# Optimization experiments

Hardware: AMD Instinct MI355X
Metric: run time of the kernel (lower is better)

Reference implementation:

```python
import jax, jax.numpy as jnp
import numpy as np

SIGMA = 4.0
KSIZE = 2 * int(4.0 * SIGMA + 0.5) + 1  # 33, as in anomalib's GaussianBlur2d
INPUT_SIZE = (224, 224)
NUM_NEIGHBORS = 9


def avg_pool_4_1_1(x):
    # nn.AvgPool2d(kernel_size=4, stride=1, padding=1), count_include_pad=True -> divide by 16
    s = jax.lax.reduce_window(x, 0.0, jax.lax.add, (1, 1, 4, 4), (1, 1, 1, 1),
                              ((0, 0), (0, 0), (1, 1), (1, 1)))
    return s / 16.0


def gaussian_kernel1d(ksize, sigma):
    x = jnp.arange(ksize, dtype=jnp.float32) - (ksize - 1) / 2.0
    g = jnp.exp(-0.5 * (x / sigma) ** 2)
    return g / jnp.sum(g)


def gaussian_blur(x):
    # separable 33x33 gaussian blur, reflect padding (kornia GaussianBlur2d default)
    k = gaussian_kernel1d(KSIZE, SIGMA)
    pad = KSIZE // 2
    xp = jnp.pad(x, ((0, 0), (0, 0), (pad, pad), (pad, pad)), mode='reflect')
    dn = ('NCHW', 'OIHW', 'NCHW')
    y = jax.lax.conv_general_dilated(xp, k.reshape(1, 1, KSIZE, 1), (1, 1), 'VALID', dimension_numbers=dn)
    y = jax.lax.conv_general_dilated(y, k.reshape(1, 1, 1, KSIZE), (1, 1), 'VALID', dimension_numbers=dn)
    return y


def euclidean_dist(x, y):
    # pairwise L2: x [..., n, d], y [..., m, d] -> [..., n, m]
    x2 = jnp.sum(x * x, axis=-1, keepdims=True)
    y2 = jnp.sum(y * y, axis=-1, keepdims=True)
    d2 = x2 - 2.0 * jnp.matmul(x, jnp.swapaxes(y, -1, -2)) + jnp.swapaxes(y2, -1, -2)
    return jnp.sqrt(jnp.clip(d2, 0.0, None))


def compute_anomaly_score(patch_scores, locations, embedding, memory_bank):
    # PatchCore re-weighting (num_neighbors > 1 branch)
    B, P = patch_scores.shape
    bidx = jnp.arange(B)
    max_patches = jnp.argmax(patch_scores, axis=1)                      # [B]
    feats = embedding.reshape(B, P, -1)[bidx, max_patches]              # [B, C]
    score = patch_scores[bidx, max_patches]                             # [B] s*
    nn_index = locations[bidx, max_patches]                             # [B]
    nn_sample = memory_bank[nn_index]                                   # [B, C]
    d_bank = euclidean_dist(nn_sample, memory_bank)                     # [B, M]
    _, support = jax.lax.top_k(-d_bank, NUM_NEIGHBORS)                  # [B, K] smallest
    support_feats = memory_bank[support]                                # [B, K, C]
    distances = euclidean_dist(feats[:, None, :], support_feats)        # [B, 1, K]
    weights = 1.0 - jnp.exp(score) / jnp.sum(jnp.exp(distances[:, 0, :]), axis=-1)
    return weights * score


def setup_inputs() -> dict:
    key = jax.random.key(0)
    k1, k2, k3 = jax.random.split(key, 3)
    feat_layer2 = jax.random.normal(k1, (8, 512, 28, 28), dtype=jnp.float32)
    feat_layer3 = jax.random.normal(k2, (8, 1024, 14, 14), dtype=jnp.float32)
    memory_bank = jax.random.normal(k3, (32000, 1536), dtype=jnp.float32)
    return {"feat_layer2": feat_layer2, "feat_layer3": feat_layer3, "memory_bank": memory_bank}


def reference(feat_layer2, feat_layer3, memory_bank):
    # feature_pooler = AvgPool2d(4,1,1)
    f2 = avg_pool_4_1_1(feat_layer2)   # [B, 512, 27, 27]
    f3 = avg_pool_4_1_1(feat_layer3)   # [B, 1024, 13, 13]
    B, _, H, W = f2.shape
    # generate_embedding: bilinear upsample layer3 to layer2 size, concat channels
    f3u = jax.image.resize(f3, (B, f3.shape[1], H, W), method='bilinear')
    emb = jnp.concatenate([f2, f3u], axis=1)                            # [B, 1536, 27, 27]
    C = emb.shape[1]
    embedding = jnp.transpose(emb, (0, 2, 3, 1)).reshape(-1, C)         # [B*H*W, C]
    # nearest_neighbors with n_neighbors=1 over the coreset memory bank
    d = euclidean_dist(embedding, memory_bank)                          # [B*H*W, M]
    patch_scores = jnp.min(d, axis=1).reshape(B, -1)
    locations = jnp.argmin(d, axis=1).reshape(B, -1)
    pred_score = compute_anomaly_score(patch_scores, locations, embedding, memory_bank)
    # anomaly map: upsample patch scores to input size + gaussian blur
    pmap = patch_scores.reshape(B, 1, H, W)
    amap = jax.image.resize(pmap, (B, 1, INPUT_SIZE[0], INPUT_SIZE[1]), method='bilinear')
    anomaly_map = gaussian_blur(amap)
    return anomaly_map, pred_score
```

## Files before the change

### kernel.cpp

```cpp
#include <hip/hip_runtime.h>
#include <math.h>

#define NB 8
#define C2 512
#define C3 1024
#define HIN2 28
#define HIN3 14
#define HO2 27
#define HO3 13
#define CC 1536
#define NP (NB*HO2*HO2)
#define NM 32000
#define NKNN 9
#define OH 224
#define AMAP_N (NB*OH*OH)

#define BM 256
#define BN 256
#define BK 64
#define KT (CC/BK)
#define MB_CNT ((NP+BM-1)/BM)
#define NB_CNT (NM/BN)
#define NWG (MB_CNT*NB_CNT)

typedef unsigned long long u64;
typedef unsigned int u32;
typedef __attribute__((ext_vector_type(8))) short bf16x8;
typedef __attribute__((ext_vector_type(4))) float f32x4;

struct GW { float w[33]; };

__device__ __forceinline__ float warp_sum(float v){
  #pragma unroll
  for (int off=32; off; off>>=1) v += __shfl_down(v, off);
  return v;
}

__device__ __forceinline__ ushort f2bf(float f){
  u32 u = __float_as_uint(f);
  u32 r = (u + 0x7FFFu + ((u>>16)&1u)) >> 16;
  return (ushort)r;
}
__device__ __forceinline__ float bf2f(ushort b){
  return __uint_as_float(((u32)b)<<16);
}

#define GLDS(g, l) __builtin_amdgcn_global_load_lds((const __attribute__((address_space(1))) void*)(g), (__attribute__((address_space(3))) void*)(l), 16, 0, 0)
#define WAITVM0() asm volatile("s_waitcnt vmcnt(0)" ::: "memory")
#define SB0() __builtin_amdgcn_sched_barrier(0)
__device__ __forceinline__ void bar_raw(){
  asm volatile("" ::: "memory");
  __builtin_amdgcn_s_barrier();
  asm volatile("" ::: "memory");
}

__global__ __launch_bounds__(256) void k_avgpool2(const float* __restrict__ in, ushort* __restrict__ embB){
  __shared__ float pl[16*789];
  int b = blockIdx.x >> 5, cg = blockIdx.x & 31;
  const float4* src = (const float4*)(in + ((size_t)b*C2 + cg*16)*(HIN2*HIN2));
  for (int idx = threadIdx.x; idx < 16*196; idx += 256){
    int c = idx/196, p4 = idx - c*196;
    float4 v = src[idx];
    float* d = &pl[c*789 + p4*4];
    d[0]=v.x; d[1]=v.y; d[2]=v.z; d[3]=v.w;
  }
  __syncthreads();
  int c = threadIdx.x & 15, g = threadIdx.x >> 4;
  for (int pos = g; pos < HO2*HO2; pos += 16){
    int i = pos/HO2, j = pos - i*HO2;
    const float* p = &pl[c*789];
    float s = 0.f;
    #pragma unroll
    for (int di=0; di<4; ++di){
      int y = i - 1 + di;
      if ((unsigned)y >= HIN2) continue;
      #pragma unroll
      for (int dj=0; dj<4; ++dj){
        int x = j - 1 + dj;
        if ((unsigned)x < HIN2) s += p[y*HIN2 + x];
      }
    }
    embB[((size_t)((b*HO2 + i)*HO2 + j))*CC + cg*16 + c] = f2bf(s * (1.f/16.f));
  }
}

__global__ __launch_bounds__(256) void k_avgpool3(const float* __restrict__ in, float* __restrict__ f3p){
  __shared__ float pl[64*197];
  int b = blockIdx.x >> 4, cg = blockIdx.x & 15;
  const float4* src = (const float4*)(in + ((size_t)b*C3 + cg*64)*(HIN3*HIN3));
  for (int idx = threadIdx.x; idx < 64*49; idx += 256){
    int c = idx/49, p4 = idx - c*49;
    float4 v = src[idx];
    float* d = &pl[c*197 + p4*4];
    d[0]=v.x; d[1]=v.y; d[2]=v.z; d[3]=v.w;
  }
  __syncthreads();
  int c = threadIdx.x & 63, g = threadIdx.x >> 6;
  for (int pos = g; pos < HO3*HO3; pos += 4){
    int i = pos/HO3, j = pos - i*HO3;
    const float* p = &pl[c*197];
    float s = 0.f;
    #pragma unroll
    for (int di=0; di<4; ++di){
      int y = i - 1 + di;
      if ((unsigned)y >= HIN3) continue;
      #pragma unroll
      for (int dj=0; dj<4; ++dj){
        int x = j - 1 + dj;
        if ((unsigned)x < HIN3) s += p[y*HIN3 + x];
      }
    }
    f3p[((size_t)((b*HO3 + i)*HO3 + j))*C3 + cg*64 + c] = s * (1.f/16.f);
  }
}

__global__ void k_upsample3(const float* __restrict__ f3p, ushort* __restrict__ embB){
  int t = blockIdx.x*256 + threadIdx.x;
  if (t >= NB*HO2*HO2*C3) return;
  int c = t % C3; int r = t / C3;
  int ox = r % HO2; r /= HO2;
  int oy = r % HO2; int b = r / HO2;
  float fy = (oy + 0.5f) * (13.f/27.f) - 0.5f;
  float fx = (ox + 0.5f) * (13.f/27.f) - 0.5f;
  int y0 = (int)floorf(fy); float wy = fy - (float)y0;
  int x0 = (int)floorf(fx); float wx = fx - (float)x0;
  int y0c = min(max(y0,0), HO3-1), y1c = min(max(y0+1,0), HO3-1);
  int x0c = min(max(x0,0), HO3-1), x1c = min(max(x0+1,0), HO3-1);
  const float* base = f3p + (size_t)(b*HO3*HO3)*C3;
  float v00 = base[(size_t)(y0c*HO3 + x0c)*C3 + c];
  float v01 = base[(size_t)(y0c*HO3 + x1c)*C3 + c];
  float v10 = base[(size_t)(y1c*HO3 + x0c)*C3 + c];
  float v11 = base[(size_t)(y1c*HO3 + x1c)*C3 + c];
  float v = (1.f-wy)*((1.f-wx)*v00 + wx*v01) + wy*((1.f-wx)*v10 + wx*v11);
  embB[((size_t)((b*HO2 + oy)*HO2 + ox))*CC + C2 + c] = f2bf(v);
}

__global__ void k_bank_prep(const float* __restrict__ bank, ushort* __restrict__ bankB,
                            float* __restrict__ y2){
  int wave = threadIdx.x >> 6, lane = threadIdx.x & 63;
  int r = blockIdx.x*4 + wave;
  if (r >= NM) return;
  const float4* p = (const float4*)(bank + (size_t)r*CC);
  ushort4* q = (ushort4*)(bankB + (size_t)r*CC);
  float s = 0.f;
  #pragma unroll
  for (int it=0; it<6; ++it){
    float4 v = p[it*64 + lane];
    s += v.x*v.x + v.y*v.y + v.z*v.z + v.w*v.w;
    ushort4 o; o.x = f2bf(v.x); o.y = f2bf(v.y); o.z = f2bf(v.z); o.w = f2bf(v.w);
    q[it*64 + lane] = o;
  }
  s = warp_sum(s);
  if (lane==0) y2[r] = s;
}

__global__ void k_rowsumsq_bf(const ushort* __restrict__ src, float* __restrict__ dst, int rows,
                              u64* __restrict__ packed){
  int wave = threadIdx.x >> 6;
  int lane = threadIdx.x & 63;
  int r = blockIdx.x*4 + wave;
  if (r >= rows) return;
  const uint4* p = (const uint4*)(src + (size_t)r*CC);
  float s = 0.f;
  #pragma unroll
  for (int it=0; it<3; ++it){
    uint4 v = p[it*64 + lane];
    u32 ws_[4] = {v.x, v.y, v.z, v.w};
    #pragma unroll
    for (int q=0;q<4;q++){
      float lo = __uint_as_float(ws_[q]<<16);
      float hi = __uint_as_float(ws_[q]&0xFFFF0000u);
      s += lo*lo + hi*hi;
    }
  }
  s = warp_sum(s);
  if (lane==0){ dst[r] = s; packed[r] = ~0ull; }
}

__global__ __launch_bounds__(512, 2) void k_distmin_mfma(
    const ushort* __restrict__ A, const ushort* __restrict__ B,
    const float* __restrict__ x2, const float* __restrict__ y2,
    u64* __restrict__ packed)
{
  __shared__ ushort smem[4*BM*BK];
  ushort* As0 = smem;
  ushort* Bs0 = smem + BM*BK;
  ushort* As1 = smem + 2*BM*BK;
  ushort* Bs1 = smem + 3*BM*BK;

  const int tid = threadIdx.x;
  const int w   = tid >> 6;
  const int l   = tid & 63;
  const int wr  = w >> 2;
  const int wc  = w & 3;
  const int ccol = l & 15;
  const int cgrp = l >> 4;

  int orig = blockIdx.x;
  const int q8 = NWG/8, r8 = NWG%8;
  int xcd = orig & 7, sidx = orig >> 3;
  int wg = (xcd < r8 ? xcd*(q8+1) : r8*(q8+1) + (xcd-r8)*q8) + sidx;
  const int mb = wg % MB_CNT;
  const int nb = wg / MB_CNT;
  const int m0 = mb * BM;
  const int n0 = nb * BN;

  const int rowin = l >> 3;
  const int scol  = (((l&7) ^ rowin) * 8);
  int chA1[2], chA2[2], chB1[2], chB2[2];
  u32 aO1[2], aO2[2], bO1[2], bO2[2];
  u32 lA1[2], lA2[2], lB1[2], lB2[2];
  #pragma unroll
  for (int c=0;c<2;c++){
    chA1[c] = (w<4) ? (2*w+c) : (8+2*w+c);
    chA2[c] = chA1[c] + 8;
    chB1[c] = (w>>1)*8 + (w&1)*2 + c;
    chB2[c] = chB1[c] + 4;
    aO1[c] = (u32)min(m0 + chA1[c]*8 + rowin, NP-1)*CC + scol;
    aO2[c] = (u32)min(m0 + chA2[c]*8 + rowin, NP-1)*CC + scol;
    bO1[c] = (u32)(n0 + chB1[c]*8 + rowin)*CC + scol;
    bO2[c] = (u32)(n0 + chB2[c]*8 + rowin)*CC + scol;
    lA1[c] = (u32)chA1[c]*1024 + l*16;
    lA2[c] = (u32)chA2[c]*1024 + l*16;
    lB1[c] = (u32)chB1[c]*1024 + l*16;
    lB2[c] = (u32)chB2[c]*1024 + l*16;
  }

  const u32 o0 = (u32)((cgrp ^ (ccol & 7)) * 8);
  u32 aRow[8], bRow[4];
  #pragma unroll
  for (int mi=0;mi<8;mi++) aRow[mi] = (u32)(wr*128 + mi*16 + ccol)*BK;
  #pragma unroll
  for (int ni=0;ni<4;ni++) bRow[ni] = (u32)(wc*64 + ni*16 + ccol)*BK;

  f32x4 acc[8][4];
  #pragma unroll
  for (int mi=0;mi<8;mi++)
    #pragma unroll
    for (int ni=0;ni<4;ni++)
      acc[mi][ni] = (f32x4){0.f,0.f,0.f,0.f};

  bf16x8 rA[8][2], rB[4][2];

  #pragma unroll
  for (int c=0;c<2;c++){
    GLDS(A + aO1[c], (char*)As0 + lA1[c]);
    GLDS(A + aO2[c], (char*)As0 + lA2[c]);
    GLDS(B + bO1[c], (char*)Bs0 + lB1[c]);
    GLDS(B + bO2[c], (char*)Bs0 + lB2[c]);
  }
  WAITVM0(); bar_raw(); SB0();
  #pragma unroll
  for (int mi=0;mi<8;mi++)
    #pragma unroll
    for (int ks=0;ks<2;ks++)
      rA[mi][ks] = *(const bf16x8*)&As0[aRow[mi] + (o0 ^ (u32)(ks<<5))];
  #pragma unroll
  for (int ni=0;ni<4;ni++)
    #pragma unroll
    for (int ks=0;ks<2;ks++)
      rB[ni][ks] = *(const bf16x8*)&Bs0[bRow[ni] + (o0 ^ (u32)(ks<<5))];

  #pragma unroll 1
  for (int kt=0; kt<KT; ++kt){
    const u32 kk = (u32)(kt+1)*BK;
    ushort* nA = (kt & 1) ? As0 : As1;
    ushort* nB = (kt & 1) ? Bs0 : Bs1;

    #pragma unroll
    for (int c=0;c<2;c++){
      GLDS(A + aO1[c] + kk, (char*)nA + lA1[c]);
      GLDS(A + aO2[c] + kk, (char*)nA + lA2[c]);
      GLDS(B + bO1[c] + kk, (char*)nB + lB1[c]);
      GLDS(B + bO2[c] + kk, (char*)nB + lB2[c]);
    }
    SB0();

    __builtin_amdgcn_s_setprio(1);
    #pragma unroll
    for (int mi=0;mi<8;mi++)
      #pragma unroll
      for (int ni=0;ni<4;ni++)
        #pragma unroll
        for (int ks=0;ks<2;ks++)
          acc[mi][ni] = __builtin_amdgcn_mfma_f32_16x16x32_bf16(rA[mi][ks], rB[ni][ks], acc[mi][ni], 0, 0, 0);
    __builtin_amdgcn_s_setprio(0);

    WAITVM0();
    bar_raw();
    SB0();

    #pragma unroll
    for (int mi=0;mi<8;mi++)
      #pragma unroll
      for (int ks=0;ks<2;ks++)
        rA[mi][ks] = *(const bf16x8*)&nA[aRow[mi] + (o0 ^ (u32)(ks<<5))];
    #pragma unroll
    for (int ni=0;ni<4;ni++)
      #pragma unroll
      for (int ks=0;ks<2;ks++)
        rB[ni][ks] = *(const bf16x8*)&nB[bRow[ni] + (o0 ^ (u32)(ks<<5))];
  }

  float xv[8][4];
  #pragma unroll
  for (int mi=0;mi<8;mi++)
    #pragma unroll
    for (int r=0;r<4;r++)
      xv[mi][r] = x2[min(m0 + wr*128 + mi*16 + cgrp*4 + r, NP-1)];

  u64 best[8][4];
  #pragma unroll
  for (int mi=0;mi<8;mi++)
    #pragma unroll
    for (int r=0;r<4;r++) best[mi][r] = ~0ull;

  #pragma unroll
  for (int ni=0;ni<4;ni++){
    const int n = n0 + wc*64 + ni*16 + ccol;
    const float yy = y2[n];
    #pragma unroll
    for (int mi=0;mi<8;mi++)
      #pragma unroll
      for (int r=0;r<4;r++){
        float d2 = fmaxf(xv[mi][r] + yy - 2.f*acc[mi][ni][r], 0.f);
        u64 pk = (((u64)__float_as_uint(d2))<<32) | (u32)n;
        if (pk < best[mi][r]) best[mi][r] = pk;
      }
  }

  #pragma unroll
  for (int mi=0;mi<8;mi++)
    #pragma unroll
    for (int r=0;r<4;r++){
      u64 pk = best[mi][r];
      #pragma unroll
      for (int md=1; md<16; md<<=1){
        u64 o = __shfl_xor(pk, md);
        if (o < pk) pk = o;
      }
      const int row = m0 + wr*128 + mi*16 + cgrp*4 + r;
      if (ccol==0 && row < NP) atomicMin(&packed[row], pk);
    }
}

__global__ void k_finalize(const u64* __restrict__ packed, float* __restrict__ patch_d,
                           int* __restrict__ sel_mp, float* __restrict__ sel_score, int* __restrict__ sel_nn){
  int b = blockIdx.x;
  int tid = threadIdx.x;
  __shared__ u64 red[4];
  u64 best = 0;
  for (int p = tid; p < HO2*HO2; p += 256){
    u64 v = packed[b*HO2*HO2 + p];
    float d = sqrtf(__uint_as_float((u32)(v>>32)));
    patch_d[b*HO2*HO2 + p] = d;
    u64 pk = (((u64)__float_as_uint(d))<<32) | (u32)(HO2*HO2 - p);
    if (pk > best) best = pk;
  }
  int lane = tid & 63, w = tid >> 6;
  #pragma unroll
  for (int d=32; d; d>>=1){ u64 o = __shfl_down(best, d); if (o > best) best = o; }
  if (lane==0) red[w] = best;
  __syncthreads();
  if (tid==0){
    u64 bb = red[0];
    for (int q=1;q<4;q++) if (red[q] > bb) bb = red[q];
    int p = HO2*HO2 - (int)(bb & 0xffffffffu);
    sel_mp[b] = p;
    sel_score[b] = __uint_as_float((u32)(bb>>32));
    sel_nn[b] = (int)(packed[b*HO2*HO2 + p] & 0xffffffffu);
  }
}

__device__ __forceinline__ void bf8dec(uint4 v, float* f){
  u32 a[4] = {v.x, v.y, v.z, v.w};
  #pragma unroll
  for (int q=0;q<4;q++){
    f[2*q]   = __uint_as_float(a[q]<<16);
    f[2*q+1] = __uint_as_float(a[q]&0xFFFF0000u);
  }
}

__global__ __launch_bounds__(256) void k_dbank(const ushort* __restrict__ bankB, const float* __restrict__ y2,
    const int* __restrict__ sel_nn, float* __restrict__ d_bank){
  int wave = threadIdx.x >> 6, lane = threadIdx.x & 63;
  int m = blockIdx.x*4 + wave;
  if (m >= NM) return;
  int nn[NB];
  #pragma unroll
  for (int b=0;b<NB;b++) nn[b] = sel_nn[b];
  const uint4* pm = (const uint4*)(bankB + (size_t)m*CC);
  float acc[NB];
  #pragma unroll
  for (int b=0;b<NB;b++) acc[b] = 0.f;
  #pragma unroll
  for (int it=0; it<3; ++it){
    uint4 v = pm[it*64 + lane];
    float vf[8]; bf8dec(v, vf);
    #pragma unroll
    for (int b=0;b<NB;b++){
      uint4 u = ((const uint4*)(bankB + (size_t)nn[b]*CC))[it*64 + lane];
      float uf[8]; bf8dec(u, uf);
      #pragma unroll
      for (int q=0;q<8;q++) acc[b] += vf[q]*uf[q];
    }
  }
  #pragma unroll
  for (int b=0;b<NB;b++){
    float s = warp_sum(acc[b]);
    if (lane==0) d_bank[(size_t)b*NM + m] = fmaxf(y2[nn[b]] + y2[m] - 2.f*s, 0.f);
  }
}

__global__ __launch_bounds__(512) void k_score(const float* __restrict__ d_bank, const float* __restrict__ bank,
    const ushort* __restrict__ embB, const float* __restrict__ x2, const float* __restrict__ y2,
    const int* __restrict__ sel_mp, const float* __restrict__ sel_score, float* __restrict__ out_score){
  int b = blockIdx.x, tid = threadIdx.x;
  __shared__ u64 cand[512*NKNN];
  __shared__ int sel[NKNN];
  __shared__ u64 red[8];
  __shared__ u64 gbest_s;
  __shared__ float fred[8];
  __shared__ float sumexp_s;

  #pragma unroll
  for (int q=0;q<NKNN;q++) cand[tid*NKNN+q] = ~0ull;
  for (int m = tid; m < NM; m += 512){
    float v = d_bank[(size_t)b*NM + m];
    u64 pk = (((u64)__float_as_uint(v))<<32) | (u32)m;
    if (pk < cand[tid*NKNN + NKNN-1]){
      cand[tid*NKNN + NKNN-1] = pk;
      for (int q=NKNN-1; q>0 && cand[tid*NKNN+q] < cand[tid*NKNN+q-1]; --q){
        u64 t = cand[tid*NKNN+q]; cand[tid*NKNN+q] = cand[tid*NKNN+q-1]; cand[tid*NKNN+q-1] = t;
      }
    }
  }
  __syncthreads();
  int lane = tid & 63, w = tid >> 6;
  for (int k=0;k<NKNN;++k){
    u64 mybest = ~0ull;
    #pragma unroll
    for (int q=0;q<NKNN;q++){ u64 v = cand[tid*NKNN+q]; if (v < mybest) mybest = v; }
    u64 rb = mybest;
    #pragma unroll
    for (int d=32; d; d>>=1){ u64 o = __shfl_down(rb, d); if (o < rb) rb = o; }
    if (lane==0) red[w] = rb;
    __syncthreads();
    if (tid==0){
      u64 bb = red[0];
      for (int q=1;q<8;q++) if (red[q] < bb) bb = red[q];
      gbest_s = bb;
      sel[k] = (int)(bb & 0xffffffffu);
    }
    __syncthreads();
    u64 gb = gbest_s;
    #pragma unroll
    for (int q=0;q<NKNN;q++) if (cand[tid*NKNN+q] == gb) cand[tid*NKNN+q] = ~0ull;
    __syncthreads();
  }

  int mp = sel_mp[b];
  const ushort* fv = embB + (size_t)(b*HO2*HO2 + mp)*CC;
  float fx2 = x2[b*HO2*HO2 + mp];
  if (tid==0) sumexp_s = 0.f;
  __syncthreads();
  for (int k=0;k<NKNN;++k){
    const float* sv = bank + (size_t)sel[k]*CC;
    float part = 0.f;
    for (int i = tid; i < CC; i += 512) part += bf2f(fv[i])*sv[i];
    part = warp_sum(part);
    if (lane==0) fred[w] = part;
    __syncthreads();
    if (tid==0){
      float dot = 0.f;
      for (int q=0;q<8;q++) dot += fred[q];
      float d2 = fmaxf(fx2 + y2[sel[k]] - 2.f*dot, 0.f);
      sumexp_s += expf(sqrtf(d2));
    }
    __syncthreads();
  }
  if (tid==0){
    float s = sel_score[b];
    out_score[b] = (1.f - expf(s)/sumexp_s) * s;
  }
}

__global__ void k_maketab(float* __restrict__ T, GW gw){
  int idx = blockIdx.x*256 + threadIdx.x;
  if (idx >= OH*HO2) return;
  int x = idx / HO2, j = idx - x*HO2;
  float s = 0.f;
  #pragma unroll
  for (int k=0;k<33;++k){
    int yy = x + k - 16;
    yy = (yy < 0) ? -yy : yy;
    yy = (yy > OH-1) ? (2*(OH-1) - yy) : yy;
    float fy = (yy + 0.5f) * (27.f/224.f) - 0.5f;
    int y0 = (int)floorf(fy); float wy = fy - (float)y0;
    int j0 = min(max(y0,0), HO2-1), j1 = min(max(y0+1,0), HO2-1);
    float c = ((j==j0)?(1.f-wy):0.f) + ((j==j1)?wy:0.f);
    s += gw.w[k]*c;
  }
  T[idx] = s;
}

__global__ __launch_bounds__(256) void k_amap_fused(const float* __restrict__ patch_d,
    const float* __restrict__ T, float* __restrict__ out){
  __shared__ float Ts[OH*HO2];
  __shared__ float ps[HO2*HO2];
  __shared__ float tmp[HO2*OH];
  int b = blockIdx.x, t = threadIdx.x;
  for (int idx=t; idx<OH*HO2; idx+=256) Ts[idx] = T[idx];
  for (int idx=t; idx<HO2*HO2; idx+=256) ps[idx] = patch_d[b*HO2*HO2+idx];
  __syncthreads();
  for (int idx=t; idx<HO2*OH; idx+=256){
    int i = idx/OH, x = idx - i*OH;
    float s = 0.f;
    #pragma unroll
    for (int j=0;j<HO2;j++) s += ps[i*HO2+j]*Ts[x*HO2+j];
    tmp[i*OH+x] = s;
  }
  __syncthreads();
  for (int idx=t; idx<OH*OH; idx+=256){
    int y = idx/OH, x = idx - y*OH;
    float s = 0.f;
    #pragma unroll
    for (int i=0;i<HO2;i++) s += Ts[y*HO2+i]*tmp[i*OH+x];
    out[(size_t)b*OH*OH + idx] = s;
  }
}

extern "C" void kernel_launch(void* const* d_in, const int* in_sizes, int n_in,
                              void* d_out, int out_size, void* d_ws, size_t ws_size,
                              hipStream_t stream){
  const float* f2   = (const float*)d_in[0];
  const float* f3   = (const float*)d_in[1];
  const float* bank = (const float*)d_in[2];
  float* out = (float*)d_out;

  char* ws = (char*)d_ws;
  size_t off = 0;
  auto alloc = [&](size_t bytes)->char*{ char* p = ws + off; off += (bytes + 255) & ~(size_t)255; return p; };
  ushort* embB    = (ushort*)alloc((size_t)NP*CC*2);
  ushort* bankB   = (ushort*)alloc((size_t)NM*CC*2);
  float* f3p      = (float*)alloc((size_t)NB*HO3*HO3*C3*4);
  float* y2       = (float*)alloc((size_t)NM*4);
  float* x2       = (float*)alloc((size_t)NP*4);
  u64*   packed   = (u64*)  alloc((size_t)NP*8);
  float* patch_d  = (float*)alloc((size_t)NP*4);
  float* d_bank   = (float*)alloc((size_t)NB*NM*4);
  int*   sel_mp   = (int*)  alloc(NB*4);
  float* sel_scr  = (float*)alloc(NB*4);
  int*   sel_nn   = (int*)  alloc(NB*4);
  float* Tmat     = (float*)alloc((size_t)OH*HO2*4);

  GW gw;
  { float s=0.f; for(int i=0;i<33;i++){ float xx=(float)i-16.f; gw.w[i]=expf(-0.5f*(xx/4.f)*(xx/4.f)); s+=gw.w[i]; }
    for(int i=0;i<33;i++) gw.w[i]/=s; }

  k_avgpool2<<<NB*32,256,0,stream>>>(f2, embB);
  k_avgpool3<<<NB*16,256,0,stream>>>(f3, f3p);
  k_upsample3<<<(NB*HO2*HO2*C3+255)/256,256,0,stream>>>(f3p, embB);
  k_bank_prep<<<(NM+3)/4,256,0,stream>>>(bank, bankB, y2);
  k_rowsumsq_bf<<<(NP+3)/4,256,0,stream>>>(embB, x2, NP, packed);
  k_maketab<<<(OH*HO2+255)/256,256,0,stream>>>(Tmat, gw);
  k_distmin_mfma<<<NWG,512,0,stream>>>(embB, bankB, x2, y2, packed);
  k_finalize<<<NB,256,0,stream>>>(packed, patch_d, sel_mp, sel_scr, sel_nn);
  k_dbank<<<(NM+3)/4,256,0,stream>>>(bankB, y2, sel_nn, d_bank);
  k_score<<<NB,512,0,stream>>>(d_bank, bank, embB, x2, y2, sel_mp, sel_scr, out + AMAP_N);
  k_amap_fused<<<NB,256,0,stream>>>(patch_d, Tmat, out);
}
```

Baseline: 941.1 us.

## Split top-9 neighbor search across many blocks and fuse blur table build

The top-9 search over the 32000-entry bank distances moves out of an 8-block kernel into a 256-block partial kernel that keeps per-thread candidates in registers, followed by a small final merge kernel. The Gaussian/bilinear table computation is folded into the anomaly-map kernel, dropping one launch. The GEMM loop also skips the out-of-range prefetch on its last k-tile. These changes target low occupancy and launch overhead in the tail stages, at the cost of an extra launch, a partial-results buffer and the table being recomputed in every block.

```diff
diff --git a/kernel.cpp b/kernel.cpp
--- a/kernel.cpp
+++ b/kernel.cpp
@@ -267,12 +267,14 @@
     ushort* nA = (kt & 1) ? As0 : As1;
     ushort* nB = (kt & 1) ? Bs0 : Bs1;
 
-    #pragma unroll
-    for (int c=0;c<2;c++){
-      GLDS(A + aO1[c] + kk, (char*)nA + lA1[c]);
-      GLDS(A + aO2[c] + kk, (char*)nA + lA2[c]);
-      GLDS(B + bO1[c] + kk, (char*)nB + lB1[c]);
-      GLDS(B + bO2[c] + kk, (char*)nB + lB2[c]);
+    if (kt+1 < KT){
+      #pragma unroll
+      for (int c=0;c<2;c++){
+        GLDS(A + aO1[c] + kk, (char*)nA + lA1[c]);
+        GLDS(A + aO2[c] + kk, (char*)nA + lA2[c]);
+        GLDS(B + bO1[c] + kk, (char*)nB + lB1[c]);
+        GLDS(B + bO2[c] + kk, (char*)nB + lB2[c]);
+      }
     }
     SB0();
 
@@ -412,35 +414,71 @@
   }
 }
 
-__global__ __launch_bounds__(512) void k_score(const float* __restrict__ d_bank, const float* __restrict__ bank,
+__global__ __launch_bounds__(256) void k_top9_part(const float* __restrict__ d_bank, u64* __restrict__ part9){
+  int b = blockIdx.x >> 5, seg = blockIdx.x & 31;
+  int tid = threadIdx.x;
+  __shared__ u64 cand[256*NKNN];
+  __shared__ u64 red[4];
+  __shared__ u64 gbest_s;
+  u64 t9[NKNN];
+  #pragma unroll
+  for (int q=0;q<NKNN;q++) t9[q] = ~0ull;
+  int base = seg*1000;
+  for (int i = tid; i < 1000; i += 256){
+    int m = base + i;
+    float v = d_bank[(size_t)b*NM + m];
+    u64 pk = (((u64)__float_as_uint(v))<<32) | (u32)m;
+    if (pk < t9[NKNN-1]){
+      t9[NKNN-1] = pk;
+      #pragma unroll
+      for (int q=NKNN-1; q>0; --q){
+        if (t9[q] < t9[q-1]){ u64 tt=t9[q]; t9[q]=t9[q-1]; t9[q-1]=tt; }
+      }
+    }
+  }
+  #pragma unroll
+  for (int q=0;q<NKNN;q++) cand[tid*NKNN+q] = t9[q];
+  __syncthreads();
+  int lane = tid & 63, w = tid >> 6;
+  for (int k=0;k<NKNN;++k){
+    u64 mybest = ~0ull;
+    #pragma unroll
+    for (int q=0;q<NKNN;q++){ u64 v = cand[tid*NKNN+q]; if (v < mybest) mybest = v; }
+    u64 rb = mybest;
+    #pragma unroll
+    for (int d=32; d; d>>=1){ u64 o = __shfl_down(rb, d); if (o < rb) rb = o; }
+    if (lane==0) red[w] = rb;
+    __syncthreads();
+    if (tid==0){
+      u64 bb = red[0];
+      for (int q=1;q<4;q++) if (red[q] < bb) bb = red[q];
+      gbest_s = bb;
+      part9[((size_t)b*32 + seg)*NKNN + k] = bb;
+    }
+    __syncthreads();
+    u64 gb = gbest_s;
+    #pragma unroll
+    for (int q=0;q<NKNN;q++) if (cand[tid*NKNN+q] == gb) cand[tid*NKNN+q] = ~0ull;
+    __syncthreads();
+  }
+}
+
+__global__ __launch_bounds__(256) void k_score_final(const u64* __restrict__ part9, const float* __restrict__ bank,
     const ushort* __restrict__ embB, const float* __restrict__ x2, const float* __restrict__ y2,
     const int* __restrict__ sel_mp, const float* __restrict__ sel_score, float* __restrict__ out_score){
   int b = blockIdx.x, tid = threadIdx.x;
-  __shared__ u64 cand[512*NKNN];
+  __shared__ u64 cand[32*NKNN];
   __shared__ int sel[NKNN];
-  __shared__ u64 red[8];
+  __shared__ u64 red[4];
   __shared__ u64 gbest_s;
-  __shared__ float fred[8];
+  __shared__ float fred[4];
   __shared__ float sumexp_s;
-
-  #pragma unroll
-  for (int q=0;q<NKNN;q++) cand[tid*NKNN+q] = ~0ull;
-  for (int m = tid; m < NM; m += 512){
-    float v = d_bank[(size_t)b*NM + m];
-    u64 pk = (((u64)__float_as_uint(v))<<32) | (u32)m;
-    if (pk < cand[tid*NKNN + NKNN-1]){
-      cand[tid*NKNN + NKNN-1] = pk;
-      for (int q=NKNN-1; q>0 && cand[tid*NKNN+q] < cand[tid*NKNN+q-1]; --q){
-        u64 t = cand[tid*NKNN+q]; cand[tid*NKNN+q] = cand[tid*NKNN+q-1]; cand[tid*NKNN+q-1] = t;
-      }
-    }
-  }
+  for (int i = tid; i < 32*NKNN; i += 256) cand[i] = part9[(size_t)b*32*NKNN + i];
   __syncthreads();
   int lane = tid & 63, w = tid >> 6;
   for (int k=0;k<NKNN;++k){
     u64 mybest = ~0ull;
-    #pragma unroll
-    for (int q=0;q<NKNN;q++){ u64 v = cand[tid*NKNN+q]; if (v < mybest) mybest = v; }
+    for (int i = tid; i < 32*NKNN; i += 256){ u64 v = cand[i]; if (v < mybest) mybest = v; }
     u64 rb = mybest;
     #pragma unroll
     for (int d=32; d; d>>=1){ u64 o = __shfl_down(rb, d); if (o < rb) rb = o; }
@@ -448,14 +486,13 @@
     __syncthreads();
     if (tid==0){
       u64 bb = red[0];
-      for (int q=1;q<8;q++) if (red[q] < bb) bb = red[q];
+      for (int q=1;q<4;q++) if (red[q] < bb) bb = red[q];
       gbest_s = bb;
       sel[k] = (int)(bb & 0xffffffffu);
     }
     __syncthreads();
     u64 gb = gbest_s;
-    #pragma unroll
-    for (int q=0;q<NKNN;q++) if (cand[tid*NKNN+q] == gb) cand[tid*NKNN+q] = ~0ull;
+    for (int i = tid; i < 32*NKNN; i += 256) if (cand[i] == gb) cand[i] = ~0ull;
     __syncthreads();
   }
 
@@ -467,13 +504,12 @@
   for (int k=0;k<NKNN;++k){
     const float* sv = bank + (size_t)sel[k]*CC;
     float part = 0.f;
-    for (int i = tid; i < CC; i += 512) part += bf2f(fv[i])*sv[i];
+    for (int i = tid; i < CC; i += 256) part += bf2f(fv[i])*sv[i];
     part = warp_sum(part);
     if (lane==0) fred[w] = part;
     __syncthreads();
     if (tid==0){
-      float dot = 0.f;
-      for (int q=0;q<8;q++) dot += fred[q];
+      float dot = fred[0]+fred[1]+fred[2]+fred[3];
       float d2 = fmaxf(fx2 + y2[sel[k]] - 2.f*dot, 0.f);
       sumexp_s += expf(sqrtf(d2));
     }
@@ -485,32 +521,28 @@
   }
 }
 
-__global__ void k_maketab(float* __restrict__ T, GW gw){
-  int idx = blockIdx.x*256 + threadIdx.x;
-  if (idx >= OH*HO2) return;
-  int x = idx / HO2, j = idx - x*HO2;
-  float s = 0.f;
-  #pragma unroll
-  for (int k=0;k<33;++k){
-    int yy = x + k - 16;
-    yy = (yy < 0) ? -yy : yy;
-    yy = (yy > OH-1) ? (2*(OH-1) - yy) : yy;
-    float fy = (yy + 0.5f) * (27.f/224.f) - 0.5f;
-    int y0 = (int)floorf(fy); float wy = fy - (float)y0;
-    int j0 = min(max(y0,0), HO2-1), j1 = min(max(y0+1,0), HO2-1);
-    float c = ((j==j0)?(1.f-wy):0.f) + ((j==j1)?wy:0.f);
-    s += gw.w[k]*c;
-  }
-  T[idx] = s;
-}
-
 __global__ __launch_bounds__(256) void k_amap_fused(const float* __restrict__ patch_d,
-    const float* __restrict__ T, float* __restrict__ out){
+    float* __restrict__ out, GW gw){
   __shared__ float Ts[OH*HO2];
   __shared__ float ps[HO2*HO2];
   __shared__ float tmp[HO2*OH];
   int b = blockIdx.x, t = threadIdx.x;
-  for (int idx=t; idx<OH*HO2; idx+=256) Ts[idx] = T[idx];
+  for (int idx=t; idx<OH*HO2; idx+=256){
+    int x = idx / HO2, j = idx - x*HO2;
+    float s = 0.f;
+    #pragma unroll
+    for (int k=0;k<33;++k){
+      int yy = x + k - 16;
+      yy = (yy < 0) ? -yy : yy;
+      yy = (yy > OH-1) ? (2*(OH-1) - yy) : yy;
+      float fy = (yy + 0.5f) * (27.f/224.f) - 0.5f;
+      int y0 = (int)floorf(fy); float wy = fy - (float)y0;
+      int j0 = min(max(y0,0), HO2-1), j1 = min(max(y0+1,0), HO2-1);
+      float c = ((j==j0)?(1.f-wy):0.f) + ((j==j1)?wy:0.f);
+      s += gw.w[k]*c;
+    }
+    Ts[idx] = s;
+  }
   for (int idx=t; idx<HO2*HO2; idx+=256) ps[idx] = patch_d[b*HO2*HO2+idx];
   __syncthreads();
   for (int idx=t; idx<HO2*OH; idx+=256){
@@ -549,10 +581,10 @@
   u64*   packed   = (u64*)  alloc((size_t)NP*8);
   float* patch_d  = (float*)alloc((size_t)NP*4);
   float* d_bank   = (float*)alloc((size_t)NB*NM*4);
+  u64*   part9    = (u64*)  alloc((size_t)NB*32*NKNN*8);
   int*   sel_mp   = (int*)  alloc(NB*4);
   float* sel_scr  = (float*)alloc(NB*4);
   int*   sel_nn   = (int*)  alloc(NB*4);
-  float* Tmat     = (float*)alloc((size_t)OH*HO2*4);
 
   GW gw;
   { float s=0.f; for(int i=0;i<33;i++){ float xx=(float)i-16.f; gw.w[i]=expf(-0.5f*(xx/4.f)*(xx/4.f)); s+=gw.w[i]; }
@@ -563,10 +595,10 @@
   k_upsample3<<<(NB*HO2*HO2*C3+255)/256,256,0,stream>>>(f3p, embB);
   k_bank_prep<<<(NM+3)/4,256,0,stream>>>(bank, bankB, y2);
   k_rowsumsq_bf<<<(NP+3)/4,256,0,stream>>>(embB, x2, NP, packed);
-  k_maketab<<<(OH*HO2+255)/256,256,0,stream>>>(Tmat, gw);
   k_distmin_mfma<<<NWG,512,0,stream>>>(embB, bankB, x2, y2, packed);
   k_finalize<<<NB,256,0,stream>>>(packed, patch_d, sel_mp, sel_scr, sel_nn);
   k_dbank<<<(NM+3)/4,256,0,stream>>>(bankB, y2, sel_nn, d_bank);
-  k_score<<<NB,512,0,stream>>>(d_bank, bank, embB, x2, y2, sel_mp, sel_scr, out + AMAP_N);
-  k_amap_fused<<<NB,256,0,stream>>>(patch_d, Tmat, out);
-}
+  k_top9_part<<<NB*32,256,0,stream>>>(d_bank, part9);
+  k_score_final<<<NB,256,0,stream>>>(part9, bank, embB, x2, y2, sel_mp, sel_scr, out + AMAP_N);
+  k_amap_fused<<<NB,256,0,stream>>>(patch_d, out, gw);
+}
```

New measurement: 944.9 us (median of 4 runs). About the same (+0.4%).
